# Performance work log

Hardware: AMD Instinct MI355X
Metric: run time of the kernel (lower is better)

Reference implementation:

```python
import jax, jax.numpy as jnp
import numpy as np

NUM_LAYERS = 2
HIDDEN = 512
INPUT = 512


def _lstm_cell(x, h, c, Wih, Whh, bih, bbh):
    # PyTorch LSTMCell: gates ordered i, f, g, o
    g = x @ Wih.T + bih + h @ Whh.T + bbh  # [B, 4H]
    i, f, gg, o = jnp.split(g, 4, axis=-1)
    c_new = jax.nn.sigmoid(f) * c + jax.nn.sigmoid(i) * jnp.tanh(gg)
    h_new = jax.nn.sigmoid(o) * jnp.tanh(c_new)
    return h_new, c_new


def setup_inputs() -> dict:
    key = jax.random.key(0)
    ks = jax.random.split(key, 8)
    B, T = 64, 512
    s = 1.0 / np.sqrt(HIDDEN)
    return {
        "x": jax.random.normal(ks[0], (B, T, INPUT), dtype=jnp.float32),
        "h0": jax.random.normal(ks[1], (NUM_LAYERS, B, HIDDEN), dtype=jnp.float32),
        "c0": jax.random.normal(ks[2], (NUM_LAYERS, B, HIDDEN), dtype=jnp.float32),
        # stacked per-layer weights (input_size == hidden_size so shapes match)
        "W_ih": jax.random.uniform(ks[3], (NUM_LAYERS, 4 * HIDDEN, INPUT), jnp.float32, -s, s),
        "W_hh": jax.random.uniform(ks[4], (NUM_LAYERS, 4 * HIDDEN, HIDDEN), jnp.float32, -s, s),
        "b_ih": jax.random.uniform(ks[5], (NUM_LAYERS, 4 * HIDDEN), jnp.float32, -s, s),
        "b_hh": jax.random.uniform(ks[6], (NUM_LAYERS, 4 * HIDDEN), jnp.float32, -s, s),
    }


def reference(x, h0, c0, W_ih, W_hh, b_ih, b_hh):
    # x: [B, T, D]; h0/c0: [L, B, H]
    xs = jnp.swapaxes(x, 0, 1)  # [T, B, D] for scan over time

    def step(carry, x_t):
        h, c = carry  # each [L, B, H]
        h_list, c_list = [], []
        inp = x_t
        for j in range(NUM_LAYERS):  # small static unroll over layers
            h_j, c_j = _lstm_cell(inp, h[j], c[j], W_ih[j], W_hh[j], b_ih[j], b_hh[j])
            h_list.append(h_j)
            c_list.append(c_j)
            inp = h_j
        h_new = jnp.stack(h_list, axis=0)
        c_new = jnp.stack(c_list, axis=0)
        return (h_new, c_new), inp  # output of top layer

    (h_fin, c_fin), outs = jax.lax.scan(step, (h0, c0), xs)
    out = jnp.swapaxes(outs, 0, 1)  # [B, T, H]
    return out, h_fin, c_fin
```

## Files before the change

### kernel.cpp

```cpp
#include <hip/hip_runtime.h>
#include <hip/hip_bf16.h>


#define TT 512

using short8 = __attribute__((ext_vector_type(8))) short;
using f32x4  = __attribute__((ext_vector_type(4))) float;

__device__ __forceinline__ short f2bf(float f) {
  unsigned u = __float_as_uint(f);
  u = (u + 0x7fffu + ((u >> 16) & 1u)) >> 16;
  return (short)u;
}
__device__ __forceinline__ float bf2f(short s) {
  return __uint_as_float(((unsigned)(unsigned short)s) << 16);
}
__device__ __forceinline__ float sigf(float x) { return 1.f / (1.f + __expf(-x)); }
__device__ __forceinline__ float tanh_(float x) { return 1.f - 2.f / (__expf(2.f * x) + 1.f); }

__device__ __forceinline__ void ld8_nw(short8* d,
    const short* p0, const short* p1, const short* p2, const short* p3,
    const short* p4, const short* p5, const short* p6, const short* p7) {
  asm volatile(
      "global_load_dwordx4 %0, %8, off sc0 sc1\n\t"
      "global_load_dwordx4 %1, %9, off sc0 sc1\n\t"
      "global_load_dwordx4 %2, %10, off sc0 sc1\n\t"
      "global_load_dwordx4 %3, %11, off sc0 sc1\n\t"
      "global_load_dwordx4 %4, %12, off sc0 sc1\n\t"
      "global_load_dwordx4 %5, %13, off sc0 sc1\n\t"
      "global_load_dwordx4 %6, %14, off sc0 sc1\n\t"
      "global_load_dwordx4 %7, %15, off sc0 sc1"
      : "=&v"(d[0]), "=&v"(d[1]), "=&v"(d[2]), "=&v"(d[3]),
        "=&v"(d[4]), "=&v"(d[5]), "=&v"(d[6]), "=&v"(d[7])
      : "v"(p0), "v"(p1), "v"(p2), "v"(p3),
        "v"(p4), "v"(p5), "v"(p6), "v"(p7)
      : "memory");
}

#define TIE8(A, CNT)                                                        \
  asm volatile(CNT : "+v"(A[0]), "+v"(A[1]), "+v"(A[2]), "+v"(A[3]),        \
                     "+v"(A[4]), "+v"(A[5]), "+v"(A[6]), "+v"(A[7])         \
               ::"memory")

__device__ __forceinline__ void stc_short(short* p, short v) {
  asm volatile("global_store_short %0, %1, off sc0 sc1"
               :: "v"(p), "v"((int)v) : "memory");
}

__global__ __launch_bounds__(256) void conv_x(const float* __restrict__ x,
                                              short* __restrict__ xo) {
  size_t g = (size_t)blockIdx.x * 256 + threadIdx.x;
  size_t i = g * 8;
  float4 v0 = *(const float4*)(x + i);
  float4 v1 = *(const float4*)(x + i + 4);
  short8 r;
  r[0] = f2bf(v0.x); r[1] = f2bf(v0.y); r[2] = f2bf(v0.z); r[3] = f2bf(v0.w);
  r[4] = f2bf(v1.x); r[5] = f2bf(v1.y); r[6] = f2bf(v1.z); r[7] = f2bf(v1.w);
  *(short8*)(xo + (i >> 9) * 1024 + (i & 511)) = r;
}

__global__ __launch_bounds__(256) void conv_w(const float* __restrict__ Wih,
                                              const float* __restrict__ Whh,
                                              short* __restrict__ wp) {
  int g = blockIdx.x * 256 + threadIdx.x;
  int l = g / 393216;
  int rem = g % 393216;
  int j8 = rem / 6144;
  int q8 = rem % 6144;
  int s, hl, bt, c, lane;
  if (q8 < 2048) {
    s = 0; hl = 0;
    int seg = q8 >> 6; bt = seg >> 4; c = seg & 15; lane = q8 & 63;
  } else {
    int q = q8 - 2048;
    s = 1;
    int seg = q >> 6; bt = seg >> 5; c = (seg >> 1) & 15; hl = seg & 1;
    lane = q & 63;
  }
  int r = lane & 15;
  int gg = r >> 2, jj = r & 3;
  int R = gg * 512 + j8 * 8 + bt * 4 + jj;
  int k = c * 32 + (lane >> 4) * 8;
  const float* src = (s ? Whh : Wih) + ((size_t)(l * 2048 + R)) * 512 + k;
  short8 o;
#pragma unroll
  for (int e = 0; e < 8; ++e) {
    float v = src[e];
    short hi = f2bf(v);
    o[e] = hl ? f2bf(v - bf2f(hi)) : hi;
  }
  *(short8*)(wp + (size_t)g * 8) = o;
}

__global__ __launch_bounds__(256) void init_state(const float* __restrict__ h0,
                                                  short* __restrict__ hhi,
                                                  short* __restrict__ hlo,
                                                  unsigned* __restrict__ bar) {
  int i = blockIdx.x * 256 + threadIdx.x;
  int l = i >> 15, bj = i & 32767;
  int b = bj >> 9, j = bj & 511;
  float h = h0[i];
  short hi = f2bf(h);
  int o = (l * 2) * 32768 + (j >> 3) * 512 + b * 8 + (j & 7);
  hhi[o] = hi;
  hlo[o] = f2bf(h - bf2f(hi));
  if (blockIdx.x < 4) bar[blockIdx.x * 256 + threadIdx.x] = 0u;
}

__device__ __forceinline__ void garrive(unsigned* bar, int tid, int slot) {
  __syncthreads();
  if (tid == 0)
    __hip_atomic_fetch_add(&bar[slot * 32], 1u, __ATOMIC_RELAXED,
                           __HIP_MEMORY_SCOPE_AGENT);
}
__device__ __forceinline__ void gwait(unsigned* bar, unsigned target, int tid) {
  if (tid == 0) {
    for (;;) {
      unsigned sum = 0;
#pragma unroll
      for (int r = 0; r < 32; ++r)
        sum += __hip_atomic_load(&bar[r * 32], __ATOMIC_RELAXED,
                                 __HIP_MEMORY_SCOPE_AGENT);
      if (sum >= target) break;
      __builtin_amdgcn_s_sleep(1);
    }
  }
  __syncthreads();
}

__global__ __launch_bounds__(512, 1) void lstm_persist(
    const short* __restrict__ wp, const float* __restrict__ c0,
    const float* __restrict__ bih, const float* __restrict__ bhh,
    short* __restrict__ hhi, short* __restrict__ hlo,
    unsigned* __restrict__ bar, float* __restrict__ out) {
  extern __shared__ char smem[];
  short* lw = (short*)smem;
  float* sG = (float*)(smem + 98304);

  const int tid = threadIdx.x;
  const int layer = blockIdx.x >> 6;
  const int j8 = blockIdx.x & 63;
  const int bslot = blockIdx.x & 31;
  const int wv = tid >> 6;
  const int kq = wv & 3;
  const int ah = wv >> 2;
  const int lane = tid & 63;
  const int m = lane & 15;
  const int koq = lane >> 4;
  const int cbase = kq << 2;

  {
    const short* src = wp + (size_t)(layer * 64 + j8) * 49152;
    for (int i = tid; i < 6144; i += 512)
      *(short8*)(lw + i * 8) = *(const short8*)(src + i * 8);
  }

  const int sb = tid >> 3, sj = tid & 7;
  const int j = (j8 << 3) + sj;
  float creg = c0[layer * 32768 + sb * 512 + j];
  float hf = 0.f;
  float bsum[4];
#pragma unroll
  for (int g = 0; g < 4; ++g)
    bsum[g] = bih[layer * 2048 + g * 512 + j] + bhh[layer * 2048 + g * 512 + j];
  __syncthreads();

  const int br0 = ((ah * 2 + 0) << 4) + m;
  const int br1 = ((ah * 2 + 1) << 4) + m;
  const short* xo = (const short*)out;

  f32x4 acc[2][2];

  auto ih_l0 = [&](int txt) {
#pragma unroll
    for (int cc = 0; cc < 4; ++cc) {
      const int c = cbase + cc;
      const int k = c * 32 + (koq << 3);
      short8 b0 = *(const short8*)(lw + c * 512 + lane * 8);
      short8 b1 = *(const short8*)(lw + (16 + c) * 512 + lane * 8);
#pragma unroll
      for (int it = 0; it < 2; ++it) {
        const int br = it ? br1 : br0;
        short8 a = *(const short8*)(xo + ((size_t)br * TT + txt) * 1024 + k);
        acc[0][it] = __builtin_amdgcn_mfma_f32_16x16x32_bf16(a, b0, acc[0][it], 0, 0, 0);
        acc[1][it] = __builtin_amdgcn_mfma_f32_16x16x32_bf16(a, b1, acc[1][it], 0, 0, 0);
      }
    }
  };

  if (layer == 0) {
#pragma unroll
    for (int u = 0; u < 2; ++u)
#pragma unroll
      for (int v = 0; v < 2; ++v) acc[u][v] = f32x4{0.f, 0.f, 0.f, 0.f};
    ih_l0(0);
  }

#define PA(rX, cc, br) \
  ((rX) + ((((cbase + (cc)) << 2) + koq) << 9) + (br) * 8)

  for (int t = 0; t <= TT; ++t) {
    const int tl = layer ? (t - 1) : t;
    if (tl >= 0 && tl < TT) {
      const int pin = tl & 1, pout = pin ^ 1;
      if (t > 0) gwait(bar, 128u * (unsigned)t, tid);

      short8 Ah[8], Al[8];
      const short* rh = hhi + (layer * 2 + pin) * 32768;
      const short* rl = hlo + (layer * 2 + pin) * 32768;

      if (layer == 0) {
        ld8_nw(Ah, PA(rh, 0, br0), PA(rh, 0, br1), PA(rh, 1, br0), PA(rh, 1, br1),
                   PA(rh, 2, br0), PA(rh, 2, br1), PA(rh, 3, br0), PA(rh, 3, br1));
        ld8_nw(Al, PA(rl, 0, br0), PA(rl, 0, br1), PA(rl, 1, br0), PA(rl, 1, br1),
                   PA(rl, 2, br0), PA(rl, 2, br1), PA(rl, 3, br0), PA(rl, 3, br1));
        TIE8(Ah, "s_waitcnt vmcnt(0)");
        TIE8(Al, "");
      } else {
#pragma unroll
        for (int u = 0; u < 2; ++u)
#pragma unroll
          for (int v = 0; v < 2; ++v) acc[u][v] = f32x4{0.f, 0.f, 0.f, 0.f};
        short8 Ax[8];
        const short* ph = hhi + (t & 1) * 32768;
        ld8_nw(Ax, PA(ph, 0, br0), PA(ph, 0, br1), PA(ph, 1, br0), PA(ph, 1, br1),
                   PA(ph, 2, br0), PA(ph, 2, br1), PA(ph, 3, br0), PA(ph, 3, br1));
        ld8_nw(Ah, PA(rh, 0, br0), PA(rh, 0, br1), PA(rh, 1, br0), PA(rh, 1, br1),
                   PA(rh, 2, br0), PA(rh, 2, br1), PA(rh, 3, br0), PA(rh, 3, br1));
        ld8_nw(Al, PA(rl, 0, br0), PA(rl, 0, br1), PA(rl, 1, br0), PA(rl, 1, br1),
                   PA(rl, 2, br0), PA(rl, 2, br1), PA(rl, 3, br0), PA(rl, 3, br1));
        TIE8(Ax, "s_waitcnt vmcnt(16)");
#pragma unroll
        for (int cc = 0; cc < 4; ++cc) {
          const int c = cbase + cc;
          short8 b0 = *(const short8*)(lw + c * 512 + lane * 8);
          short8 b1 = *(const short8*)(lw + (16 + c) * 512 + lane * 8);
#pragma unroll
          for (int it = 0; it < 2; ++it) {
            short8 a = Ax[cc * 2 + it];
            acc[0][it] = __builtin_amdgcn_mfma_f32_16x16x32_bf16(a, b0, acc[0][it], 0, 0, 0);
            acc[1][it] = __builtin_amdgcn_mfma_f32_16x16x32_bf16(a, b1, acc[1][it], 0, 0, 0);
          }
        }
        TIE8(Ah, "s_waitcnt vmcnt(0)");
        TIE8(Al, "");
      }

#pragma unroll
      for (int cc = 0; cc < 4; ++cc) {
        const int c = cbase + cc;
        short8 bh0 = *(const short8*)(lw + 16384 + (c * 2 + 0) * 512 + lane * 8);
        short8 bl0 = *(const short8*)(lw + 16384 + (c * 2 + 1) * 512 + lane * 8);
        short8 bh1 = *(const short8*)(lw + 16384 + ((16 + c) * 2 + 0) * 512 + lane * 8);
        short8 bl1 = *(const short8*)(lw + 16384 + ((16 + c) * 2 + 1) * 512 + lane * 8);
#pragma unroll
        for (int it = 0; it < 2; ++it) {
          short8 a = Ah[cc * 2 + it];
          short8 al = Al[cc * 2 + it];
          acc[0][it] = __builtin_amdgcn_mfma_f32_16x16x32_bf16(a, bh0, acc[0][it], 0, 0, 0);
          acc[0][it] = __builtin_amdgcn_mfma_f32_16x16x32_bf16(a, bl0, acc[0][it], 0, 0, 0);
          acc[0][it] = __builtin_amdgcn_mfma_f32_16x16x32_bf16(al, bh0, acc[0][it], 0, 0, 0);
          acc[1][it] = __builtin_amdgcn_mfma_f32_16x16x32_bf16(a, bh1, acc[1][it], 0, 0, 0);
          acc[1][it] = __builtin_amdgcn_mfma_f32_16x16x32_bf16(a, bl1, acc[1][it], 0, 0, 0);
          acc[1][it] = __builtin_amdgcn_mfma_f32_16x16x32_bf16(al, bh1, acc[1][it], 0, 0, 0);
        }
      }

#pragma unroll
      for (int bt = 0; bt < 2; ++bt)
#pragma unroll
        for (int it = 0; it < 2; ++it) {
          const int srow = bt * 16 + m;
          const int col = ((ah * 2 + it) << 4) + (koq << 2);
#pragma unroll
          for (int r = 0; r < 4; ++r)
            sG[(kq * 32 + srow) * 66 + col + r] = acc[bt][it][r];
        }
      __syncthreads();

      {
        const int bt = sj >> 2, jl = sj & 3;
        float gv[4];
#pragma unroll
        for (int g = 0; g < 4; ++g) {
          const int s = bt * 16 + g * 4 + jl;
          gv[g] = sG[(0 * 32 + s) * 66 + sb] + sG[(1 * 32 + s) * 66 + sb] +
                  sG[(2 * 32 + s) * 66 + sb] + sG[(3 * 32 + s) * 66 + sb] +
                  bsum[g];
        }
        const float cn = sigf(gv[1]) * creg + sigf(gv[0]) * tanh_(gv[2]);
        const float hn = sigf(gv[3]) * tanh_(cn);
        creg = cn;
        hf = hn;
        const int ho = (layer * 2 + pout) * 32768 + (j8 << 9) + tid;
        const short hb = f2bf(hn);
        stc_short(hhi + ho, hb);
        stc_short(hlo + ho, f2bf(hn - bf2f(hb)));
        if (layer)
          __builtin_nontemporal_store(hn, &out[((size_t)sb * 512 + tl) * 512 + j]);
      }
    }
    if (t < TT) {
      garrive(bar, tid, bslot);
      if (layer == 0 && t + 1 < TT) {
#pragma unroll
        for (int u = 0; u < 2; ++u)
#pragma unroll
          for (int v = 0; v < 2; ++v) acc[u][v] = f32x4{0.f, 0.f, 0.f, 0.f};
        ih_l0(t + 1);
      }
    }
  }

  out[16777216 + layer * 32768 + sb * 512 + j] = hf;
  out[16777216 + 65536 + layer * 32768 + sb * 512 + j] = creg;
}


extern "C" void kernel_launch(void* const* d_in, const int* in_sizes, int n_in,
                              void* d_out, int out_size, void* d_ws,
                              size_t ws_size, hipStream_t stream) {
  const float* x = (const float*)d_in[0];
  const float* h0 = (const float*)d_in[1];
  const float* c0 = (const float*)d_in[2];
  const float* Wih = (const float*)d_in[3];
  const float* Whh = (const float*)d_in[4];
  const float* bih = (const float*)d_in[5];
  const float* bhh = (const float*)d_in[6];
  float* out = (float*)d_out;

  char* ws = (char*)d_ws;
  short* wp = (short*)(ws + 0);
  short* hhi = (short*)(ws + 12582912);
  short* hlo = (short*)(ws + 12845056);
  unsigned* bar = (unsigned*)(ws + 13107200);

  hipFuncSetAttribute(reinterpret_cast<const void*>(lstm_persist),
                      hipFuncAttributeMaxDynamicSharedMemorySize, 132096);

  conv_x<<<8192, 256, 0, stream>>>(x, (short*)out);
  conv_w<<<3072, 256, 0, stream>>>(Wih, Whh, wp);
  init_state<<<256, 256, 0, stream>>>(h0, hhi, hlo, bar);

  void* args[] = {(void*)&wp,  (void*)&c0,  (void*)&bih, (void*)&bhh,
                  (void*)&hhi, (void*)&hlo, (void*)&bar, (void*)&out};
  hipLaunchCooperativeKernel(reinterpret_cast<void*>(lstm_persist), dim3(128),
                             dim3(512), args, 132096, stream);
}
```

Before: 2.760 ms.

## Decouple layer barriers with per-layer counters and ring-buffered hidden state

The single global barrier shared by both layers is split into two per-layer arrival counters. Layer 0 keeps a 4-slot ring of h and may run up to three steps ahead of layer 1. Layer 1 waits only on its own peers plus layer 0's progress, and computes its input projection for the next step right after arriving. This loosens the lockstep coupling between layers so each layer's critical path is no longer gated by the other's step latency. The cost is more workspace and extra counter polling per wait.

```diff
diff --git a/kernel.cpp b/kernel.cpp
--- a/kernel.cpp
+++ b/kernel.cpp
@@ -101,27 +101,46 @@
   int b = bj >> 9, j = bj & 511;
   float h = h0[i];
   short hi = f2bf(h);
-  int o = (l * 2) * 32768 + (j >> 3) * 512 + b * 8 + (j & 7);
+  int slot = l ? 5 : 3;
+  int o = slot * 32768 + (j >> 3) * 512 + b * 8 + (j & 7);
   hhi[o] = hi;
   hlo[o] = f2bf(h - bf2f(hi));
-  if (blockIdx.x < 4) bar[blockIdx.x * 256 + threadIdx.x] = 0u;
-}
-
-__device__ __forceinline__ void garrive(unsigned* bar, int tid, int slot) {
+  if (blockIdx.x < 8) bar[blockIdx.x * 256 + threadIdx.x] = 0u;
+}
+
+__device__ __forceinline__ void garrive(unsigned* cnt, int tid, int slot) {
   __syncthreads();
   if (tid == 0)
-    __hip_atomic_fetch_add(&bar[slot * 32], 1u, __ATOMIC_RELAXED,
+    __hip_atomic_fetch_add(&cnt[slot * 32], 1u, __ATOMIC_RELAXED,
                            __HIP_MEMORY_SCOPE_AGENT);
 }
-__device__ __forceinline__ void gwait(unsigned* bar, unsigned target, int tid) {
+__device__ __forceinline__ void gwait1(unsigned* c1, unsigned t1, int tid) {
   if (tid == 0) {
     for (;;) {
-      unsigned sum = 0;
+      unsigned s1 = 0;
 #pragma unroll
       for (int r = 0; r < 32; ++r)
-        sum += __hip_atomic_load(&bar[r * 32], __ATOMIC_RELAXED,
-                                 __HIP_MEMORY_SCOPE_AGENT);
-      if (sum >= target) break;
+        s1 += __hip_atomic_load(&c1[r * 32], __ATOMIC_RELAXED,
+                                __HIP_MEMORY_SCOPE_AGENT);
+      if (s1 >= t1) break;
+      __builtin_amdgcn_s_sleep(1);
+    }
+  }
+  __syncthreads();
+}
+__device__ __forceinline__ void gwait2(unsigned* c1, unsigned t1,
+                                       unsigned* c2, unsigned t2, int tid) {
+  if (tid == 0) {
+    for (;;) {
+      unsigned s1 = 0, s2 = 0;
+#pragma unroll
+      for (int r = 0; r < 32; ++r) {
+        s1 += __hip_atomic_load(&c1[r * 32], __ATOMIC_RELAXED,
+                                __HIP_MEMORY_SCOPE_AGENT);
+        s2 += __hip_atomic_load(&c2[r * 32], __ATOMIC_RELAXED,
+                                __HIP_MEMORY_SCOPE_AGENT);
+      }
+      if (s1 >= t1 && s2 >= t2) break;
       __builtin_amdgcn_s_sleep(1);
     }
   }
@@ -141,6 +160,8 @@
   const int layer = blockIdx.x >> 6;
   const int j8 = blockIdx.x & 63;
   const int bslot = blockIdx.x & 31;
+  unsigned* cntMy = bar + (layer << 10);
+  unsigned* cntOt = bar + ((layer ^ 1) << 10);
   const int wv = tid >> 6;
   const int kq = wv & 3;
   const int ah = wv >> 2;
@@ -171,6 +192,16 @@
 
   f32x4 acc[2][2];
 
+  auto zacc = [&]() {
+#pragma unroll
+    for (int u = 0; u < 2; ++u)
+#pragma unroll
+      for (int v = 0; v < 2; ++v) acc[u][v] = f32x4{0.f, 0.f, 0.f, 0.f};
+  };
+
+#define PA(rX, cc, br) \
+  ((rX) + ((((cbase + (cc)) << 2) + koq) << 9) + (br) * 8)
+
   auto ih_l0 = [&](int txt) {
 #pragma unroll
     for (int cc = 0; cc < 4; ++cc) {
@@ -188,126 +219,118 @@
     }
   };
 
+  auto ih_l1 = [&](const short* ph) {
+    short8 Ax[8];
+    ld8_nw(Ax, PA(ph, 0, br0), PA(ph, 0, br1), PA(ph, 1, br0), PA(ph, 1, br1),
+               PA(ph, 2, br0), PA(ph, 2, br1), PA(ph, 3, br0), PA(ph, 3, br1));
+    TIE8(Ax, "s_waitcnt vmcnt(0)");
+#pragma unroll
+    for (int cc = 0; cc < 4; ++cc) {
+      const int c = cbase + cc;
+      short8 b0 = *(const short8*)(lw + c * 512 + lane * 8);
+      short8 b1 = *(const short8*)(lw + (16 + c) * 512 + lane * 8);
+#pragma unroll
+      for (int it = 0; it < 2; ++it) {
+        short8 a = Ax[cc * 2 + it];
+        acc[0][it] = __builtin_amdgcn_mfma_f32_16x16x32_bf16(a, b0, acc[0][it], 0, 0, 0);
+        acc[1][it] = __builtin_amdgcn_mfma_f32_16x16x32_bf16(a, b1, acc[1][it], 0, 0, 0);
+      }
+    }
+  };
+
+  auto stepBody = [&](const short* rh, const short* rl, int slotOut, int t) {
+    short8 Ah[8], Al[8];
+    ld8_nw(Ah, PA(rh, 0, br0), PA(rh, 0, br1), PA(rh, 1, br0), PA(rh, 1, br1),
+               PA(rh, 2, br0), PA(rh, 2, br1), PA(rh, 3, br0), PA(rh, 3, br1));
+    ld8_nw(Al, PA(rl, 0, br0), PA(rl, 0, br1), PA(rl, 1, br0), PA(rl, 1, br1),
+               PA(rl, 2, br0), PA(rl, 2, br1), PA(rl, 3, br0), PA(rl, 3, br1));
+    TIE8(Ah, "s_waitcnt vmcnt(0)");
+    TIE8(Al, "");
+
+#pragma unroll
+    for (int cc = 0; cc < 4; ++cc) {
+      const int c = cbase + cc;
+      short8 bh0 = *(const short8*)(lw + 16384 + (c * 2 + 0) * 512 + lane * 8);
+      short8 bl0 = *(const short8*)(lw + 16384 + (c * 2 + 1) * 512 + lane * 8);
+      short8 bh1 = *(const short8*)(lw + 16384 + ((16 + c) * 2 + 0) * 512 + lane * 8);
+      short8 bl1 = *(const short8*)(lw + 16384 + ((16 + c) * 2 + 1) * 512 + lane * 8);
+#pragma unroll
+      for (int it = 0; it < 2; ++it) {
+        short8 a = Ah[cc * 2 + it];
+        short8 al = Al[cc * 2 + it];
+        acc[0][it] = __builtin_amdgcn_mfma_f32_16x16x32_bf16(a, bh0, acc[0][it], 0, 0, 0);
+        acc[0][it] = __builtin_amdgcn_mfma_f32_16x16x32_bf16(a, bl0, acc[0][it], 0, 0, 0);
+        acc[0][it] = __builtin_amdgcn_mfma_f32_16x16x32_bf16(al, bh0, acc[0][it], 0, 0, 0);
+        acc[1][it] = __builtin_amdgcn_mfma_f32_16x16x32_bf16(a, bh1, acc[1][it], 0, 0, 0);
+        acc[1][it] = __builtin_amdgcn_mfma_f32_16x16x32_bf16(a, bl1, acc[1][it], 0, 0, 0);
+        acc[1][it] = __builtin_amdgcn_mfma_f32_16x16x32_bf16(al, bh1, acc[1][it], 0, 0, 0);
+      }
+    }
+
+#pragma unroll
+    for (int bt = 0; bt < 2; ++bt)
+#pragma unroll
+      for (int it = 0; it < 2; ++it) {
+        const int srow = bt * 16 + m;
+        const int col = ((ah * 2 + it) << 4) + (koq << 2);
+#pragma unroll
+        for (int r = 0; r < 4; ++r)
+          sG[(kq * 32 + srow) * 66 + col + r] = acc[bt][it][r];
+      }
+    __syncthreads();
+
+    {
+      const int bt = sj >> 2, jl = sj & 3;
+      float gv[4];
+#pragma unroll
+      for (int g = 0; g < 4; ++g) {
+        const int s = bt * 16 + g * 4 + jl;
+        gv[g] = sG[(0 * 32 + s) * 66 + sb] + sG[(1 * 32 + s) * 66 + sb] +
+                sG[(2 * 32 + s) * 66 + sb] + sG[(3 * 32 + s) * 66 + sb] +
+                bsum[g];
+      }
+      const float cn = sigf(gv[1]) * creg + sigf(gv[0]) * tanh_(gv[2]);
+      const float hn = sigf(gv[3]) * tanh_(cn);
+      creg = cn;
+      hf = hn;
+      const int ho = slotOut * 32768 + (j8 << 9) + tid;
+      const short hb = f2bf(hn);
+      stc_short(hhi + ho, hb);
+      stc_short(hlo + ho, f2bf(hn - bf2f(hb)));
+      if (layer)
+        __builtin_nontemporal_store(hn, &out[((size_t)sb * 512 + t) * 512 + j]);
+    }
+  };
+
   if (layer == 0) {
-#pragma unroll
-    for (int u = 0; u < 2; ++u)
-#pragma unroll
-      for (int v = 0; v < 2; ++v) acc[u][v] = f32x4{0.f, 0.f, 0.f, 0.f};
+    zacc();
     ih_l0(0);
-  }
-
-#define PA(rX, cc, br) \
-  ((rX) + ((((cbase + (cc)) << 2) + koq) << 9) + (br) * 8)
-
-  for (int t = 0; t <= TT; ++t) {
-    const int tl = layer ? (t - 1) : t;
-    if (tl >= 0 && tl < TT) {
-      const int pin = tl & 1, pout = pin ^ 1;
-      if (t > 0) gwait(bar, 128u * (unsigned)t, tid);
-
-      short8 Ah[8], Al[8];
-      const short* rh = hhi + (layer * 2 + pin) * 32768;
-      const short* rl = hlo + (layer * 2 + pin) * 32768;
-
-      if (layer == 0) {
-        ld8_nw(Ah, PA(rh, 0, br0), PA(rh, 0, br1), PA(rh, 1, br0), PA(rh, 1, br1),
-                   PA(rh, 2, br0), PA(rh, 2, br1), PA(rh, 3, br0), PA(rh, 3, br1));
-        ld8_nw(Al, PA(rl, 0, br0), PA(rl, 0, br1), PA(rl, 1, br0), PA(rl, 1, br1),
-                   PA(rl, 2, br0), PA(rl, 2, br1), PA(rl, 3, br0), PA(rl, 3, br1));
-        TIE8(Ah, "s_waitcnt vmcnt(0)");
-        TIE8(Al, "");
-      } else {
-#pragma unroll
-        for (int u = 0; u < 2; ++u)
-#pragma unroll
-          for (int v = 0; v < 2; ++v) acc[u][v] = f32x4{0.f, 0.f, 0.f, 0.f};
-        short8 Ax[8];
-        const short* ph = hhi + (t & 1) * 32768;
-        ld8_nw(Ax, PA(ph, 0, br0), PA(ph, 0, br1), PA(ph, 1, br0), PA(ph, 1, br1),
-                   PA(ph, 2, br0), PA(ph, 2, br1), PA(ph, 3, br0), PA(ph, 3, br1));
-        ld8_nw(Ah, PA(rh, 0, br0), PA(rh, 0, br1), PA(rh, 1, br0), PA(rh, 1, br1),
-                   PA(rh, 2, br0), PA(rh, 2, br1), PA(rh, 3, br0), PA(rh, 3, br1));
-        ld8_nw(Al, PA(rl, 0, br0), PA(rl, 0, br1), PA(rl, 1, br0), PA(rl, 1, br1),
-                   PA(rl, 2, br0), PA(rl, 2, br1), PA(rl, 3, br0), PA(rl, 3, br1));
-        TIE8(Ax, "s_waitcnt vmcnt(16)");
-#pragma unroll
-        for (int cc = 0; cc < 4; ++cc) {
-          const int c = cbase + cc;
-          short8 b0 = *(const short8*)(lw + c * 512 + lane * 8);
-          short8 b1 = *(const short8*)(lw + (16 + c) * 512 + lane * 8);
-#pragma unroll
-          for (int it = 0; it < 2; ++it) {
-            short8 a = Ax[cc * 2 + it];
-            acc[0][it] = __builtin_amdgcn_mfma_f32_16x16x32_bf16(a, b0, acc[0][it], 0, 0, 0);
-            acc[1][it] = __builtin_amdgcn_mfma_f32_16x16x32_bf16(a, b1, acc[1][it], 0, 0, 0);
-          }
-        }
-        TIE8(Ah, "s_waitcnt vmcnt(0)");
-        TIE8(Al, "");
-      }
-
-#pragma unroll
-      for (int cc = 0; cc < 4; ++cc) {
-        const int c = cbase + cc;
-        short8 bh0 = *(const short8*)(lw + 16384 + (c * 2 + 0) * 512 + lane * 8);
-        short8 bl0 = *(const short8*)(lw + 16384 + (c * 2 + 1) * 512 + lane * 8);
-        short8 bh1 = *(const short8*)(lw + 16384 + ((16 + c) * 2 + 0) * 512 + lane * 8);
-        short8 bl1 = *(const short8*)(lw + 16384 + ((16 + c) * 2 + 1) * 512 + lane * 8);
-#pragma unroll
-        for (int it = 0; it < 2; ++it) {
-          short8 a = Ah[cc * 2 + it];
-          short8 al = Al[cc * 2 + it];
-          acc[0][it] = __builtin_amdgcn_mfma_f32_16x16x32_bf16(a, bh0, acc[0][it], 0, 0, 0);
-          acc[0][it] = __builtin_amdgcn_mfma_f32_16x16x32_bf16(a, bl0, acc[0][it], 0, 0, 0);
-          acc[0][it] = __builtin_amdgcn_mfma_f32_16x16x32_bf16(al, bh0, acc[0][it], 0, 0, 0);
-          acc[1][it] = __builtin_amdgcn_mfma_f32_16x16x32_bf16(a, bh1, acc[1][it], 0, 0, 0);
-          acc[1][it] = __builtin_amdgcn_mfma_f32_16x16x32_bf16(a, bl1, acc[1][it], 0, 0, 0);
-          acc[1][it] = __builtin_amdgcn_mfma_f32_16x16x32_bf16(al, bh1, acc[1][it], 0, 0, 0);
-        }
-      }
-
-#pragma unroll
-      for (int bt = 0; bt < 2; ++bt)
-#pragma unroll
-        for (int it = 0; it < 2; ++it) {
-          const int srow = bt * 16 + m;
-          const int col = ((ah * 2 + it) << 4) + (koq << 2);
-#pragma unroll
-          for (int r = 0; r < 4; ++r)
-            sG[(kq * 32 + srow) * 66 + col + r] = acc[bt][it][r];
-        }
-      __syncthreads();
-
-      {
-        const int bt = sj >> 2, jl = sj & 3;
-        float gv[4];
-#pragma unroll
-        for (int g = 0; g < 4; ++g) {
-          const int s = bt * 16 + g * 4 + jl;
-          gv[g] = sG[(0 * 32 + s) * 66 + sb] + sG[(1 * 32 + s) * 66 + sb] +
-                  sG[(2 * 32 + s) * 66 + sb] + sG[(3 * 32 + s) * 66 + sb] +
-                  bsum[g];
-        }
-        const float cn = sigf(gv[1]) * creg + sigf(gv[0]) * tanh_(gv[2]);
-        const float hn = sigf(gv[3]) * tanh_(cn);
-        creg = cn;
-        hf = hn;
-        const int ho = (layer * 2 + pout) * 32768 + (j8 << 9) + tid;
-        const short hb = f2bf(hn);
-        stc_short(hhi + ho, hb);
-        stc_short(hlo + ho, f2bf(hn - bf2f(hb)));
-        if (layer)
-          __builtin_nontemporal_store(hn, &out[((size_t)sb * 512 + tl) * 512 + j]);
-      }
-    }
-    if (t < TT) {
-      garrive(bar, tid, bslot);
-      if (layer == 0 && t + 1 < TT) {
-#pragma unroll
-        for (int u = 0; u < 2; ++u)
-#pragma unroll
-          for (int v = 0; v < 2; ++v) acc[u][v] = f32x4{0.f, 0.f, 0.f, 0.f};
+    for (int t = 0; t < TT; ++t) {
+      if (t >= 4)
+        gwait2(cntMy, (unsigned)(64 * t), cntOt, (unsigned)(64 * (t - 3)), tid);
+      else if (t >= 1)
+        gwait1(cntMy, (unsigned)(64 * t), tid);
+      const int ps = (t + 3) & 3;
+      stepBody(hhi + ps * 32768, hlo + ps * 32768, t & 3, t);
+      garrive(cntMy, tid, bslot);
+      if (t + 1 < TT) {
+        zacc();
         ih_l0(t + 1);
+      }
+    }
+  } else {
+    zacc();
+    gwait1(cntOt, 64u, tid);
+    ih_l1(hhi + 0 * 32768);
+    for (int t = 0; t < TT; ++t) {
+      if (t >= 1) gwait1(cntMy, (unsigned)(64 * t), tid);
+      const int ps = 4 + ((t + 1) & 1);
+      stepBody(hhi + ps * 32768, hlo + ps * 32768, 4 + (t & 1), t);
+      garrive(cntMy, tid, bslot);
+      if (t + 1 < TT) {
+        gwait1(cntOt, (unsigned)(64 * (t + 2)), tid);
+        zacc();
+        ih_l1(hhi + ((t + 1) & 3) * 32768);
       }
     }
   }
@@ -332,8 +355,8 @@
   char* ws = (char*)d_ws;
   short* wp = (short*)(ws + 0);
   short* hhi = (short*)(ws + 12582912);
-  short* hlo = (short*)(ws + 12845056);
-  unsigned* bar = (unsigned*)(ws + 13107200);
+  short* hlo = (short*)(ws + 12976128);
+  unsigned* bar = (unsigned*)(ws + 13369344);
 
   hipFuncSetAttribute(reinterpret_cast<const void*>(lstm_persist),
                       hipFuncAttributeMaxDynamicSharedMemorySize, 132096);
```

New measurement: 2.801 ms. Within noise of the previous version (+1.5%).
